# Kernel tuning notes

Hardware: AMD Instinct MI355X
Metric: run time of the kernel (lower is better)

Reference implementation:

```python
import jax, jax.numpy as jnp
import numpy as np

N_NODES = 50000
N_EDGES = 800000
IN_DIM = 128
HIDDEN = 64
NEG_SLOPE = 0.2


def setup_inputs() -> dict:
    key = jax.random.key(0)
    ks = jax.random.split(key, 8)
    x = jax.random.normal(ks[0], (N_NODES, IN_DIM), dtype=jnp.float32)
    edge_index = jax.random.randint(ks[1], (2, N_EDGES), 0, N_NODES, dtype=jnp.int64)
    # GATConv params (heads=1)
    W = jax.random.normal(ks[2], (HIDDEN, IN_DIM), dtype=jnp.float32) / np.sqrt(IN_DIM)
    att_src = jax.random.normal(ks[3], (HIDDEN,), dtype=jnp.float32) / np.sqrt(HIDDEN)
    att_dst = jax.random.normal(ks[4], (HIDDEN,), dtype=jnp.float32) / np.sqrt(HIDDEN)
    bias_conv = jnp.zeros((HIDDEN,), dtype=jnp.float32)
    # final Linear(hidden, 1)
    W_lin = jax.random.normal(ks[5], (1, HIDDEN), dtype=jnp.float32) / np.sqrt(HIDDEN)
    b_lin = jnp.zeros((1,), dtype=jnp.float32)
    return {"x": x, "edge_index": edge_index, "W": W, "att_src": att_src,
            "att_dst": att_dst, "bias_conv": bias_conv, "W_lin": W_lin, "b_lin": b_lin}


def _gat_forward(x, edge_index, W, att_src, att_dst, bias_conv, W_lin, b_lin):
    n = x.shape[0]
    # add self-loops (PyG GATConv default)
    loop = jnp.arange(n, dtype=edge_index.dtype)
    src = jnp.concatenate([edge_index[0], loop])  # source nodes j (messages from)
    dst = jnp.concatenate([edge_index[1], loop])  # destination nodes i (aggregated at)

    h = x @ W.T                                   # [N, H] projected features
    a_src = h @ att_src                           # [N]
    a_dst = h @ att_dst                           # [N]

    e = jax.nn.leaky_relu(a_src[src] + a_dst[dst], NEG_SLOPE)  # [E']
    # segment softmax over incoming edges of each destination node
    m = jax.ops.segment_max(e, dst, num_segments=n)            # [N]
    ex = jnp.exp(e - m[dst])
    s = jax.ops.segment_sum(ex, dst, num_segments=n)           # [N]
    alpha = ex / s[dst]                                        # [E']

    out = jax.ops.segment_sum(alpha[:, None] * h[src], dst, num_segments=n)
    out = out + bias_conv                         # [N, H]

    out = jax.nn.relu(out)
    # dropout p=0.5 is a no-op in eval mode
    y = jax.nn.sigmoid(out @ W_lin.T + b_lin)     # [N, 1]
    return y


def reference(x, edge_index, W, att_src, att_dst, bias_conv, W_lin, b_lin):
    return _gat_forward(x, edge_index, W, att_src, att_dst, bias_conv, W_lin, b_lin)
```

## Files before the change

### kernel.cpp

```cpp
#include <hip/hip_runtime.h>
#include <hip/hip_bf16.h>
#include <hip/hip_fp16.h>
#include <cstdint>

#define IND 128
#define HID 64
#define NEG_SLOPE 0.2f
#define EPB 4096
#define CBSHIFT 8
#define BCAP 8192
#define SORT_THREADS 256
#define EPT (EPB / SORT_THREADS)
#define HBCAP 4096

__device__ __forceinline__ unsigned short f2bf_bits(float f) {
  __hip_bfloat16 b = __float2bfloat16(f);
  return *reinterpret_cast<unsigned short*>(&b);
}
__device__ __forceinline__ unsigned short f2h_bits(float f) {
  __half h = __float2half(f);
  return *reinterpret_cast<unsigned short*>(&h);
}
__device__ __forceinline__ float h2f_bits(unsigned short u) {
  __half_raw r; r.x = u;
  return __half2float(__half(r));
}
__device__ __forceinline__ float bf2f_bits(unsigned short u) {
  return __uint_as_float((unsigned)u << 16);
}
__device__ __forceinline__ unsigned pack_bf2(float lo, float hi) {
  return (unsigned)f2bf_bits(lo) | ((unsigned)f2bf_bits(hi) << 16);
}
__device__ __forceinline__ float bf_lo(unsigned u) {
  return __uint_as_float(u << 16);
}
__device__ __forceinline__ float bf_hi(unsigned u) {
  return __uint_as_float(u & 0xFFFF0000u);
}

__global__ __launch_bounds__(256) void k_proj_sort(
    const float* __restrict__ x, const float* __restrict__ W,
    const float* __restrict__ att_s, const float* __restrict__ att_d,
    unsigned short* __restrict__ h, float* __restrict__ a_src,
    float* __restrict__ a_dst,
    const int* __restrict__ ei, int* __restrict__ gcur,
    unsigned* __restrict__ tmp, int E, long long E2,
    int nSort, int nbuck, int n)
{
  __shared__ __align__(16) char smem[49664];
  const int tid = threadIdx.x;

  if (blockIdx.x < (unsigned)nSort) {
    int* hist       = (int*)smem;
    int* sums       = hist + 256;
    int* cur        = sums + 256;
    int* gbase      = cur + 256;
    unsigned* sorted = (unsigned*)(gbase + 256);

    hist[tid] = 0;
    __syncthreads();

    const long long i0 = (long long)blockIdx.x * EPB;

    unsigned pk[EPT];
#pragma unroll
    for (int j = 0; j < EPT; ++j) {
      long long idx = i0 + j * SORT_THREADS + tid;
      unsigned v = 0xFFFFFFFFu;
      if (idx < E2) {
        int s, d;
        if (idx < E) { s = ei[idx]; d = ei[E + idx]; }
        else         { s = d = (int)(idx - E); }
        v = ((unsigned)d << 16) | (unsigned)s;
        atomicAdd(&hist[d >> CBSHIFT], 1);
      }
      pk[j] = v;
    }
    __syncthreads();

    sums[tid] = hist[tid];
    __syncthreads();
    for (int off = 1; off < 256; off <<= 1) {
      int t = (tid >= off) ? sums[tid - off] : 0;
      __syncthreads();
      sums[tid] += t;
      __syncthreads();
    }
    {
      const int lstart_t = sums[tid] - hist[tid];
      cur[tid] = lstart_t;
      gbase[tid] = (tid < nbuck && hist[tid] > 0)
                     ? tid * BCAP + atomicAdd(&gcur[tid], hist[tid]) : 0;
    }
    __syncthreads();
    hist[tid] = sums[tid] - hist[tid];
    __syncthreads();

#pragma unroll
    for (int j = 0; j < EPT; ++j) {
      unsigned v = pk[j];
      if (v != 0xFFFFFFFFu) {
        int b = v >> (16 + CBSHIFT);
        int lpos = atomicAdd(&cur[b], 1);
        sorted[lpos] = v;
      }
    }
    __syncthreads();

    const int cntE = (int)((E2 - i0 < EPB) ? (E2 - i0) : EPB);
    for (int i = tid; i < cntE; i += SORT_THREADS) {
      unsigned v = sorted[i];
      int b = v >> (16 + CBSHIFT);
      tmp[gbase[b] + (i - hist[b])] = v;
    }
    return;
  }

  float*    xs   = (float*)smem;
  unsigned* wt   = (unsigned*)(smem + 32768);
  float*    sa_l = (float*)(smem + 49152);
  float*    sd_l = (float*)(smem + 49408);

  const int nodeBase = (blockIdx.x - nSort) * 64;

  if (tid < 64) { sa_l[tid] = 0.f; sd_l[tid] = 0.f; }

#pragma unroll
  for (int it = 0; it < 4; ++it) {
    int fi = (it * 256 + tid) * 8;
    int row = fi >> 7, k = fi & 127;
    float4 w0 = *(const float4*)(W + fi);
    float4 w1 = *(const float4*)(W + fi + 4);
    uint4 pv;
    pv.x = pack_bf2(w0.x, w0.y);
    pv.y = pack_bf2(w0.z, w0.w);
    pv.z = pack_bf2(w1.x, w1.y);
    pv.w = pack_bf2(w1.z, w1.w);
    int c = (k >> 3) ^ ((row >> 2) & 7);
    ((uint4*)wt)[row * 16 + c] = pv;
  }
#pragma unroll
  for (int it = 0; it < 8; ++it) {
    int fi = (it * 256 + tid) * 4;
    int nl = fi >> 7, k = fi & 127;
    int ks = k ^ (((nl >> 2) & 7) << 2);
    int node = nodeBase + nl; if (node >= n) node = n - 1;
    float4 v = *(const float4*)(x + (size_t)node * IND + k);
    *(float4*)&xs[nl * 128 + ks] = v;
  }
  __syncthreads();

  const int ng = tid & 15;
  const int hg = tid >> 4;
  const int swzA = (ng & 7) << 2;
  const int swzB = hg & 7;
  const float* xrow0 = &xs[(4 * ng) * 128];
  const uint4* wrow0 = ((const uint4*)wt) + (4 * hg) * 16;

  float acc[4][4];
#pragma unroll
  for (int j = 0; j < 4; ++j)
#pragma unroll
    for (int i = 0; i < 4; ++i) acc[j][i] = 0.f;

  for (int k = 0; k < IND; k += 8) {
    float4 a0[4], a1[4];
#pragma unroll
    for (int j = 0; j < 4; ++j) {
      a0[j] = *(const float4*)(xrow0 + j * 128 + (k ^ swzA));
      a1[j] = *(const float4*)(xrow0 + j * 128 + ((k + 4) ^ swzA));
    }
    uint4 bw[4];
#pragma unroll
    for (int i = 0; i < 4; ++i)
      bw[i] = wrow0[i * 16 + ((k >> 3) ^ swzB)];

#pragma unroll
    for (int i = 0; i < 4; ++i) {
      float b0 = bf_lo(bw[i].x), b1 = bf_hi(bw[i].x);
      float b2 = bf_lo(bw[i].y), b3 = bf_hi(bw[i].y);
      float b4 = bf_lo(bw[i].z), b5 = bf_hi(bw[i].z);
      float b6 = bf_lo(bw[i].w), b7 = bf_hi(bw[i].w);
#pragma unroll
      for (int j = 0; j < 4; ++j) {
        acc[j][i] = fmaf(a0[j].x, b0, acc[j][i]);
        acc[j][i] = fmaf(a0[j].y, b1, acc[j][i]);
        acc[j][i] = fmaf(a0[j].z, b2, acc[j][i]);
        acc[j][i] = fmaf(a0[j].w, b3, acc[j][i]);
        acc[j][i] = fmaf(a1[j].x, b4, acc[j][i]);
        acc[j][i] = fmaf(a1[j].y, b5, acc[j][i]);
        acc[j][i] = fmaf(a1[j].z, b6, acc[j][i]);
        acc[j][i] = fmaf(a1[j].w, b7, acc[j][i]);
      }
    }
  }

#pragma unroll
  for (int j = 0; j < 4; ++j) {
    int node = nodeBase + 4 * ng + j;
    if (node < n) {
      ushort4 hv;
      hv.x = f2bf_bits(acc[j][0]);
      hv.y = f2bf_bits(acc[j][1]);
      hv.z = f2bf_bits(acc[j][2]);
      hv.w = f2bf_bits(acc[j][3]);
      *(ushort4*)(h + (size_t)node * HID + 4 * hg) = hv;
    }
  }

  float4 as4 = *(const float4*)(att_s + 4 * hg);
  float4 ad4 = *(const float4*)(att_d + 4 * hg);
#pragma unroll
  for (int j = 0; j < 4; ++j) {
    float ps = acc[j][0]*as4.x + acc[j][1]*as4.y + acc[j][2]*as4.z + acc[j][3]*as4.w;
    float pd = acc[j][0]*ad4.x + acc[j][1]*ad4.y + acc[j][2]*ad4.z + acc[j][3]*ad4.w;
    ps += __shfl_xor(ps, 16, 64); ps += __shfl_xor(ps, 32, 64);
    pd += __shfl_xor(pd, 16, 64); pd += __shfl_xor(pd, 32, 64);
    if ((tid & 63) < 16) {
      atomicAdd(&sa_l[4 * ng + j], ps);
      atomicAdd(&sd_l[4 * ng + j], pd);
    }
  }
  __syncthreads();
  if (tid < 64) {
    int node = nodeBase + tid;
    if (node < n) { a_src[node] = sa_l[tid]; a_dst[node] = sd_l[tid]; }
  }
}

__global__ __launch_bounds__(1024) void k_csr_gather(
    const unsigned* __restrict__ tmp, const int* __restrict__ gcur,
    const float* __restrict__ a_src, const float* __restrict__ a_dst,
    const unsigned short* __restrict__ h,
    const float* __restrict__ bias, const float* __restrict__ W_lin,
    const float* __restrict__ b_lin, float* __restrict__ y, int n)
{
  __shared__ int degl[128], sums[128], cur[128];
  __shared__ float adl[128];
  __shared__ unsigned csrw[HBCAP];

  const int tid  = threadIdx.x;
  const int blk  = blockIdx.x;
  const int b    = blk >> 1;
  const int n0   = (b << CBSHIFT) + ((blk & 1) << 7);
  const int base = b * BCAP;
  const int next = base + gcur[b];

  if (tid < 128) {
    degl[tid] = 0;
    const int node = n0 + tid;
    adl[tid] = (node < n) ? a_dst[node] : 0.f;
  }
  __syncthreads();

  for (int i = base + tid; i < next; i += 1024) {
    unsigned dl = (tmp[i] >> 16) - (unsigned)n0;
    if (dl < 128u) atomicAdd(&degl[dl], 1);
  }
  __syncthreads();

  if (tid < 128) sums[tid] = degl[tid];
  __syncthreads();
  for (int off = 1; off < 128; off <<= 1) {
    int t = (tid >= off && tid < 128) ? sums[tid - off] : 0;
    __syncthreads();
    if (tid < 128) sums[tid] += t;
    __syncthreads();
  }
  if (tid < 128) cur[tid] = sums[tid] - degl[tid];
  __syncthreads();

  for (int i = base + tid; i < next; i += 1024) {
    unsigned v = tmp[i];
    unsigned dl = (v >> 16) - (unsigned)n0;
    if (dl < 128u) {
      int s = (int)(v & 0xFFFFu);
      float sc = a_src[s] + adl[dl];
      sc = (sc >= 0.f) ? sc : NEG_SLOPE * sc;
      float w = expf(sc);
      int pos = atomicAdd(&cur[dl], 1);
      csrw[pos] = (unsigned)s | ((unsigned)f2h_bits(w) << 16);
    }
  }
  __syncthreads();

  const int lane    = tid & 63;
  const int wid     = tid >> 6;
  const int quarter = lane >> 4;
  const int sub     = lane & 15;

  for (int nl = wid; nl < 128; nl += 16) {
    const int node = n0 + nl;
    if (node >= n) break;

    const int dg  = degl[nl];
    const int rsl = sums[nl] - dg;

    float wpart = 0.f;
    float acc0 = 0.f, acc1 = 0.f, acc2 = 0.f, acc3 = 0.f;

    for (int bb = 0; bb < dg; bb += 64) {
      int i = bb + lane;
      unsigned pk = (i < dg) ? csrw[rsl + i] : 0u;
      wpart += h2f_bits((unsigned short)(pk >> 16));
      const int cnt = (dg - bb < 64) ? (dg - bb) : 64;

      int j = 0;
      for (; j + 8 <= cnt; j += 8) {
#pragma unroll
        for (int g = 0; g < 2; ++g) {
          int e = j + 4 * g + quarter;
          unsigned pe = __shfl(pk, e, 64);
          float we = h2f_bits((unsigned short)(pe >> 16));
          unsigned se = pe & 0xFFFFu;
          ushort4 hb = ((const ushort4*)(h + (size_t)se * HID))[sub];
          acc0 = fmaf(we, bf2f_bits(hb.x), acc0);
          acc1 = fmaf(we, bf2f_bits(hb.y), acc1);
          acc2 = fmaf(we, bf2f_bits(hb.z), acc2);
          acc3 = fmaf(we, bf2f_bits(hb.w), acc3);
        }
      }
      for (; j < cnt; j += 4) {
        int e = j + quarter;
        bool val = e < cnt;
        unsigned pe = __shfl(pk, val ? e : 0, 64);
        float we = val ? h2f_bits((unsigned short)(pe >> 16)) : 0.f;
        unsigned se = val ? (pe & 0xFFFFu) : 0u;
        ushort4 hb = ((const ushort4*)(h + (size_t)se * HID))[sub];
        acc0 = fmaf(we, bf2f_bits(hb.x), acc0);
        acc1 = fmaf(we, bf2f_bits(hb.y), acc1);
        acc2 = fmaf(we, bf2f_bits(hb.z), acc2);
        acc3 = fmaf(we, bf2f_bits(hb.w), acc3);
      }
    }

    acc0 += __shfl_xor(acc0, 16, 64); acc0 += __shfl_xor(acc0, 32, 64);
    acc1 += __shfl_xor(acc1, 16, 64); acc1 += __shfl_xor(acc1, 32, 64);
    acc2 += __shfl_xor(acc2, 16, 64); acc2 += __shfl_xor(acc2, 32, 64);
    acc3 += __shfl_xor(acc3, 16, 64); acc3 += __shfl_xor(acc3, 32, 64);

    float wsum = wpart;
#pragma unroll
    for (int o = 32; o; o >>= 1) wsum += __shfl_xor(wsum, o, 64);
    const float inv = 1.f / wsum;

    float4 bb4 = ((const float4*)bias)[sub];
    float4 ww  = ((const float4*)W_lin)[sub];
    float v0 = fmaxf(acc0 * inv + bb4.x, 0.f);
    float v1 = fmaxf(acc1 * inv + bb4.y, 0.f);
    float v2 = fmaxf(acc2 * inv + bb4.z, 0.f);
    float v3 = fmaxf(acc3 * inv + bb4.w, 0.f);
    float z = v0 * ww.x + v1 * ww.y + v2 * ww.z + v3 * ww.w;
#pragma unroll
    for (int o = 8; o; o >>= 1) z += __shfl_xor(z, o, 64);
    if (lane == 0)
      y[node] = 1.f / (1.f + expf(-(z + b_lin[0])));
  }
}


extern "C" void kernel_launch(void* const* d_in, const int* in_sizes, int n_in,
                              void* d_out, int out_size, void* d_ws, size_t ws_size,
                              hipStream_t stream)
{
  const float* x     = (const float*)d_in[0];
  const int*   ei    = (const int*)d_in[1];
  const float* W     = (const float*)d_in[2];
  const float* att_s = (const float*)d_in[3];
  const float* att_d = (const float*)d_in[4];
  const float* bias  = (const float*)d_in[5];
  const float* W_lin = (const float*)d_in[6];
  const float* b_lin = (const float*)d_in[7];
  float* y = (float*)d_out;

  const int n = in_sizes[0] / IND;
  const int E = in_sizes[1] / 2;
  const long long E2 = (long long)E + n;
  const int nSort = (int)((E2 + EPB - 1) / EPB);
  const int nProj = (n + 63) / 64;
  const int nbuck = (n + (1 << CBSHIFT) - 1) >> CBSHIFT;

  char* ws = (char*)d_ws;
  unsigned short* h = (unsigned short*)ws; ws += (size_t)n * HID * sizeof(unsigned short);
  float*    a_src  = (float*)ws;    ws += (size_t)n * sizeof(float);
  float*    a_dst  = (float*)ws;    ws += (size_t)n * sizeof(float);
  int*      gcur   = (int*)ws;      ws += (size_t)nbuck * sizeof(int);
  unsigned* tmp    = (unsigned*)ws; ws += (size_t)nbuck * BCAP * sizeof(unsigned);

  hipMemsetAsync(gcur, 0, (size_t)nbuck * sizeof(int), stream);

  k_proj_sort<<<nSort + nProj, 256, 0, stream>>>(
      x, W, att_s, att_d, h, a_src, a_dst,
      ei, gcur, tmp, E, E2, nSort, nbuck, n);

  k_csr_gather<<<nbuck * 2, 1024, 0, stream>>>(
      tmp, gcur, a_src, a_dst, h, bias, W_lin, b_lin, y, n);
}
```

Baseline: 135.8 us.

## Split gather into quarter-bucket blocks and cache bucket entries in registers

Each 256-node bucket is now handled by four 512-thread blocks of 64 nodes instead of two 1024-thread blocks of 128 nodes, halving the per-block shared CSR buffer. The bucket's packed edges are read once into a register array and reused for both the degree count and the scatter pass, so the second global read of the bucket is gone. The aim is more blocks in flight and less global traffic. In exchange each block still scans the whole bucket, so total scan work doubles, and edges past the 2048-entry per-quarter cap are silently dropped.

```diff
diff --git a/kernel.cpp b/kernel.cpp
--- a/kernel.cpp
+++ b/kernel.cpp
@@ -11,7 +11,9 @@
 #define BCAP 8192
 #define SORT_THREADS 256
 #define EPT (EPB / SORT_THREADS)
-#define HBCAP 4096
+#define QCAP 2048
+#define GT 512
+#define GSCAN (BCAP / GT)
 
 __device__ __forceinline__ unsigned short f2bf_bits(float f) {
   __hip_bfloat16 b = __float2bfloat16(f);
@@ -228,58 +230,70 @@
   }
 }
 
-__global__ __launch_bounds__(1024) void k_csr_gather(
+__global__ __launch_bounds__(GT) void k_csr_gather(
     const unsigned* __restrict__ tmp, const int* __restrict__ gcur,
     const float* __restrict__ a_src, const float* __restrict__ a_dst,
     const unsigned short* __restrict__ h,
     const float* __restrict__ bias, const float* __restrict__ W_lin,
     const float* __restrict__ b_lin, float* __restrict__ y, int n)
 {
-  __shared__ int degl[128], sums[128], cur[128];
-  __shared__ float adl[128];
-  __shared__ unsigned csrw[HBCAP];
+  __shared__ int degl[64], sums[64], cur[64];
+  __shared__ float adl[64];
+  __shared__ unsigned csrw[QCAP];
 
   const int tid  = threadIdx.x;
   const int blk  = blockIdx.x;
-  const int b    = blk >> 1;
-  const int n0   = (b << CBSHIFT) + ((blk & 1) << 7);
+  const int b    = blk >> 2;
+  const int n0   = (b << CBSHIFT) + ((blk & 3) << 6);
   const int base = b * BCAP;
   const int next = base + gcur[b];
 
-  if (tid < 128) {
+  if (tid < 64) {
     degl[tid] = 0;
     const int node = n0 + tid;
     adl[tid] = (node < n) ? a_dst[node] : 0.f;
   }
   __syncthreads();
 
-  for (int i = base + tid; i < next; i += 1024) {
-    unsigned dl = (tmp[i] >> 16) - (unsigned)n0;
-    if (dl < 128u) atomicAdd(&degl[dl], 1);
-  }
-  __syncthreads();
-
-  if (tid < 128) sums[tid] = degl[tid];
-  __syncthreads();
-  for (int off = 1; off < 128; off <<= 1) {
-    int t = (tid >= off && tid < 128) ? sums[tid - off] : 0;
-    __syncthreads();
-    if (tid < 128) sums[tid] += t;
-    __syncthreads();
-  }
-  if (tid < 128) cur[tid] = sums[tid] - degl[tid];
-  __syncthreads();
-
-  for (int i = base + tid; i < next; i += 1024) {
-    unsigned v = tmp[i];
-    unsigned dl = (v >> 16) - (unsigned)n0;
-    if (dl < 128u) {
+  unsigned pkv[GSCAN];
+#pragma unroll
+  for (int j = 0; j < GSCAN; ++j) {
+    int i = base + j * GT + tid;
+    unsigned v = 0xFFFFFFFFu;
+    if (i < next) {
+      v = tmp[i];
+      unsigned dl = (v >> 16) - (unsigned)n0;
+      if (dl < 64u) atomicAdd(&degl[dl], 1);
+      else v = 0xFFFFFFFFu;
+    }
+    pkv[j] = v;
+  }
+  __syncthreads();
+
+  if (tid == 0 && sums != nullptr) {}
+  if (tid < 64) sums[tid] = degl[tid];
+  __syncthreads();
+  for (int off = 1; off < 64; off <<= 1) {
+    int t = (tid >= off && tid < 64) ? sums[tid - off] : 0;
+    __syncthreads();
+    if (tid < 64) sums[tid] += t;
+    __syncthreads();
+  }
+  if (tid < 64) cur[tid] = sums[tid] - degl[tid];
+  __syncthreads();
+
+#pragma unroll
+  for (int j = 0; j < GSCAN; ++j) {
+    unsigned v = pkv[j];
+    if (v != 0xFFFFFFFFu) {
+      unsigned dl = (v >> 16) - (unsigned)n0;
       int s = (int)(v & 0xFFFFu);
       float sc = a_src[s] + adl[dl];
       sc = (sc >= 0.f) ? sc : NEG_SLOPE * sc;
       float w = expf(sc);
       int pos = atomicAdd(&cur[dl], 1);
-      csrw[pos] = (unsigned)s | ((unsigned)f2h_bits(w) << 16);
+      if (pos < QCAP)
+        csrw[pos] = (unsigned)s | ((unsigned)f2h_bits(w) << 16);
     }
   }
   __syncthreads();
@@ -289,12 +303,14 @@
   const int quarter = lane >> 4;
   const int sub     = lane & 15;
 
-  for (int nl = wid; nl < 128; nl += 16) {
+  for (int nl = wid; nl < 64; nl += 8) {
     const int node = n0 + nl;
     if (node >= n) break;
 
-    const int dg  = degl[nl];
-    const int rsl = sums[nl] - dg;
+    int rsl = sums[nl] - degl[nl];
+    int dg  = degl[nl];
+    if (rsl + dg > QCAP) dg = (QCAP > rsl) ? (QCAP - rsl) : 0;
+    if (rsl >= QCAP) { rsl = 0; dg = 0; }
 
     float wpart = 0.f;
     float acc0 = 0.f, acc1 = 0.f, acc2 = 0.f, acc3 = 0.f;
@@ -393,6 +409,6 @@
       x, W, att_s, att_d, h, a_src, a_dst,
       ei, gcur, tmp, E, E2, nSort, nbuck, n);
 
-  k_csr_gather<<<nbuck * 2, 1024, 0, stream>>>(
+  k_csr_gather<<<nbuck * 4, GT, 0, stream>>>(
       tmp, gcur, a_src, a_dst, h, bias, W_lin, b_lin, y, n);
 }
```

After: 136.8 us. No clear change (+0.7%).
